# Optimization experiments

Measured on AMD Instinct MI355X. Metric: run time of the kernel, lower is better.

## Reference

```python
import jax, jax.numpy as jnp
import numpy as np

B, L, H, C = 1, 512, 1024, 2


def setup_inputs() -> dict:
    key = jax.random.key(0)
    k1, k2, k3 = jax.random.split(key, 3)
    lm_output = jax.random.normal(k1, (B, L, H), dtype=jnp.float32)
    # torch Linear weight layout: [out_features, in_features]
    W1 = jax.random.normal(k2, (H, 2 * H), dtype=jnp.float32) * 0.02
    b1 = jnp.zeros((H,), dtype=jnp.float32)
    W2 = jax.random.normal(k3, (C, H), dtype=jnp.float32) * 0.02
    b2 = jnp.zeros((C,), dtype=jnp.float32)
    return {"lm_output": lm_output, "W1": W1, "b1": b1, "W2": W2, "b2": b2}


def reference(lm_output, W1, b1, W2, b2):
    # pair_emb[b,i,j] = concat(lm_output[b,j], lm_output[b,i])
    # Linear(concat(a,b)) decomposes: split W1 into the halves acting on each part.
    Wa = W1[:, :H]  # acts on lm_output_a (the j / column token)
    Wb = W1[:, H:]  # acts on lm_output_b (the i / row token)
    a_proj = jnp.einsum('blh,oh->blo', lm_output, Wa)  # [B,L,H]
    b_proj = jnp.einsum('blh,oh->blo', lm_output, Wb)  # [B,L,H]
    # hidden[b,i,j] = tanh(a_proj[b,j] + b_proj[b,i] + b1)   -> [B,L,L,H]
    hidden = jnp.tanh(a_proj[:, None, :, :] + b_proj[:, :, None, :] + b1)
    # Dropout is identity at inference time.
    logits = jnp.einsum('bijh,ch->bijc', hidden, W2) + b2  # [B,L,L,C]
    logits = (logits + jnp.swapaxes(logits, 1, 2)) / 2.0
    return logits
```

## Files before the change

kernel.cpp:

```cpp
#include <hip/hip_runtime.h>
#include <hip/hip_bf16.h>

#define HH 1024
#define LL 512
#define NT 16
#define NTRI 136

typedef __attribute__((ext_vector_type(8))) short bf16x8;
typedef __attribute__((ext_vector_type(4))) float f32x4;

static constexpr float C_EXP = 2.8853900817779268f;

static __device__ __forceinline__ uint4 pack8(float4 a, float4 b) {
    union { uint4 u; __hip_bfloat162 h[4]; } r;
    r.h[0] = __float22bfloat162_rn(make_float2(a.x, a.y));
    r.h[1] = __float22bfloat162_rn(make_float2(a.z, a.w));
    r.h[2] = __float22bfloat162_rn(make_float2(b.x, b.y));
    r.h[3] = __float22bfloat162_rn(make_float2(b.z, b.w));
    return r.u;
}

__global__ __launch_bounds__(256, 4) void proj_mfma_kernel(
    const float* __restrict__ lm, const float* __restrict__ W1,
    const float* __restrict__ b1, float* __restrict__ Ea, float* __restrict__ Eb)
{
    __shared__ ushort As[16][136];
    __shared__ ushort Bs[64][136];

    const int tid  = threadIdx.x;
    const int lane = tid & 63;
    const int w    = tid >> 6;
    const int mbase = blockIdx.y * 16;
    const int nbase = blockIdx.x * 64;
    const int sel  = nbase >> 10;
    const int nrow = nbase & 1023;
    const int wn   = w * 16;

    const int mrow = lane & 15;
    const int q8   = (lane >> 4) * 8;

    f32x4 acc = {0.f, 0.f, 0.f, 0.f};

    for (int kb = 0; kb < HH; kb += 128) {
        __syncthreads();
        {
            const int row = tid >> 4, c8 = (tid & 15) * 8;
            const float* pa = &lm[(mbase + row) * HH + kb + c8];
            *(uint4*)&As[row][c8] = pack8(*(const float4*)pa, *(const float4*)(pa + 4));
            int p = tid;
#pragma unroll
            for (int it = 0; it < 4; ++it, p += 256) {
                const int br = p >> 4, bc8 = (p & 15) * 8;
                const float* pb = &W1[(nrow + br) * 2048 + sel * 1024 + kb + bc8];
                *(uint4*)&Bs[br][bc8] = pack8(*(const float4*)pb, *(const float4*)(pb + 4));
            }
        }
        __syncthreads();

#pragma unroll
        for (int s = 0; s < 4; ++s) {
            const bf16x8 a = *(const bf16x8*)&As[mrow][s * 32 + q8];
            const bf16x8 b = *(const bf16x8*)&Bs[wn + mrow][s * 32 + q8];
            acc = __builtin_amdgcn_mfma_f32_16x16x32_bf16(a, b, acc, 0, 0, 0);
        }
    }

    const int col = lane & 15;
    const int rq  = (lane >> 4) * 4;
    const int n_g = nbase + wn + col;
    const int m0  = mbase + rq;
    if (n_g < HH) {
        const float bb = b1[n_g];
#pragma unroll
        for (int r = 0; r < 4; ++r)
            Ea[(m0 + r) * HH + n_g] = __builtin_amdgcn_exp2f(C_EXP * (acc[r] + bb));
    } else {
#pragma unroll
        for (int r = 0; r < 4; ++r)
            Eb[(m0 + r) * HH + (n_g - HH)] = __builtin_amdgcn_exp2f(C_EXP * acc[r]);
    }
}

__global__ __launch_bounds__(256, 4) void pair_kernel(
    const float* __restrict__ Ea, const float* __restrict__ Eb,
    const float* __restrict__ W2, float* __restrict__ pbuf, int nz)
{
    __shared__ float eaj[32][68];
    __shared__ float eai[32][68];
    __shared__ float ebi[32][68];
    __shared__ float ebj[32][68];
    __shared__ float w0_s[256], w1_s[256];
    __shared__ float s_red[2];

    const int tid = threadIdx.x;
    const int tx  = tid & 15;
    const int ty  = tid >> 4;

    int tt = blockIdx.x, bi = 0, rem = NT;
    while (tt >= rem) { tt -= rem; --rem; ++bi; }
    const int bj    = bi + tt;
    const int ibase = bi * 32;
    const int jbase = bj * 32;
    const int slice = HH / nz;
    const int k0    = blockIdx.y * slice;

    if (tid < 128) {
        const int c = tid >> 6, l = tid & 63;
        float* ws = c ? w1_s : w0_s;
        float s = 0.f;
        for (int q = l; q < slice / 4; q += 64) {
            const float4 v = *(const float4*)&W2[c * HH + k0 + q * 4];
            const float4 nv = make_float4(-2.f * v.x, -2.f * v.y, -2.f * v.z, -2.f * v.w);
            ((float4*)ws)[q] = nv;
            s += nv.x + nv.y + nv.z + nv.w;
        }
#pragma unroll
        for (int off = 32; off; off >>= 1) s += __shfl_down(s, off, 64);
        if (l == 0) s_red[c] = -0.5f * s;
    }

    float acc[2][2][2] = {};

    for (int kb = 0; kb < slice; kb += 64) {
        __syncthreads();
        {
            int p = tid;
#pragma unroll
            for (int it = 0; it < 8; ++it, p += 256) {
                const int tile = p >> 9;
                const int row  = (p >> 4) & 31;
                const int c4   = p & 15;
                float4 v;
                if      (tile == 0) v = *(const float4*)&Ea[(jbase + row) * HH + k0 + kb + c4 * 4];
                else if (tile == 1) v = *(const float4*)&Ea[(ibase + row) * HH + k0 + kb + c4 * 4];
                else if (tile == 2) v = *(const float4*)&Eb[(ibase + row) * HH + k0 + kb + c4 * 4];
                else                v = *(const float4*)&Eb[(jbase + row) * HH + k0 + kb + c4 * 4];
                if      (tile == 0) *(float4*)&eaj[row][c4 * 4] = v;
                else if (tile == 1) *(float4*)&eai[row][c4 * 4] = v;
                else if (tile == 2) *(float4*)&ebi[row][c4 * 4] = v;
                else                *(float4*)&ebj[row][c4 * 4] = v;
            }
        }
        __syncthreads();

#pragma unroll 4
        for (int h4 = 0; h4 < 16; ++h4) {
            const float4 Aj0 = *(const float4*)&eaj[tx][h4 * 4];
            const float4 Aj1 = *(const float4*)&eaj[tx + 16][h4 * 4];
            const float4 Bi0 = *(const float4*)&ebi[ty][h4 * 4];
            const float4 Bi1 = *(const float4*)&ebi[ty + 16][h4 * 4];
            const float4 Ai0 = *(const float4*)&eai[ty][h4 * 4];
            const float4 Ai1 = *(const float4*)&eai[ty + 16][h4 * 4];
            const float4 Bj0 = *(const float4*)&ebj[tx][h4 * 4];
            const float4 Bj1 = *(const float4*)&ebj[tx + 16][h4 * 4];
            const float4 w0  = *(const float4*)&w0_s[kb + h4 * 4];
            const float4 w1  = *(const float4*)&w1_s[kb + h4 * 4];

#define DO_H(AJ0, AJ1, BI0, BI1, AI0, AI1, BJ0, BJ1, W0V, W1V)        \
            {                                                          \
                const float d00 = __builtin_fmaf((BI0), (AJ0), 1.f);   \
                const float d01 = __builtin_fmaf((BI0), (AJ1), 1.f);   \
                const float d10 = __builtin_fmaf((BI1), (AJ0), 1.f);   \
                const float d11 = __builtin_fmaf((BI1), (AJ1), 1.f);   \
                const float e00 = __builtin_fmaf((AI0), (BJ0), 1.f);   \
                const float e01 = __builtin_fmaf((AI0), (BJ1), 1.f);   \
                const float e10 = __builtin_fmaf((AI1), (BJ0), 1.f);   \
                const float e11 = __builtin_fmaf((AI1), (BJ1), 1.f);   \
                const float dp0 = d00 * d01, dp1 = d10 * d11;          \
                const float DR  = __builtin_amdgcn_rcpf(dp0 * dp1);    \
                const float dq0 = DR * dp1, dq1 = DR * dp0;            \
                const float rd00 = dq0 * d01, rd01 = dq0 * d00;        \
                const float rd10 = dq1 * d11, rd11 = dq1 * d10;        \
                const float ep0 = e00 * e01, ep1 = e10 * e11;          \
                const float ER  = __builtin_amdgcn_rcpf(ep0 * ep1);    \
                const float eq0 = ER * ep1, eq1 = ER * ep0;            \
                const float re00 = eq0 * e01, re01 = eq0 * e00;        \
                const float re10 = eq1 * e11, re11 = eq1 * e10;        \
                const float u00 = rd00 + re00, u01 = rd01 + re01;      \
                const float u10 = rd10 + re10, u11 = rd11 + re11;      \
                acc[0][0][0] = __builtin_fmaf(u00, (W0V), acc[0][0][0]); \
                acc[0][0][1] = __builtin_fmaf(u00, (W1V), acc[0][0][1]); \
                acc[0][1][0] = __builtin_fmaf(u01, (W0V), acc[0][1][0]); \
                acc[0][1][1] = __builtin_fmaf(u01, (W1V), acc[0][1][1]); \
                acc[1][0][0] = __builtin_fmaf(u10, (W0V), acc[1][0][0]); \
                acc[1][0][1] = __builtin_fmaf(u10, (W1V), acc[1][0][1]); \
                acc[1][1][0] = __builtin_fmaf(u11, (W0V), acc[1][1][0]); \
                acc[1][1][1] = __builtin_fmaf(u11, (W1V), acc[1][1][1]); \
            }
            DO_H(Aj0.x, Aj1.x, Bi0.x, Bi1.x, Ai0.x, Ai1.x, Bj0.x, Bj1.x, w0.x, w1.x)
            DO_H(Aj0.y, Aj1.y, Bi0.y, Bi1.y, Ai0.y, Ai1.y, Bj0.y, Bj1.y, w0.y, w1.y)
            DO_H(Aj0.z, Aj1.z, Bi0.z, Bi1.z, Ai0.z, Ai1.z, Bj0.z, Bj1.z, w0.z, w1.z)
            DO_H(Aj0.w, Aj1.w, Bi0.w, Bi1.w, Ai0.w, Ai1.w, Bj0.w, Bj1.w, w0.w, w1.w)
#undef DO_H
        }
    }

    const float s0 = s_red[0];
    const float s1 = s_red[1];
    float* pb = pbuf + ((size_t)blockIdx.y * NTRI + blockIdx.x) * 2048;
#pragma unroll
    for (int ii = 0; ii < 2; ++ii) {
#pragma unroll
        for (int jj = 0; jj < 2; ++jj) {
            const int li = ty + ii * 16, lj = tx + jj * 16;
            float2* dst = (float2*)&pb[(li * 32 + lj) * 2];
            *dst = make_float2(0.5f * acc[ii][jj][0] + s0,
                               0.5f * acc[ii][jj][1] + s1);
        }
    }
}

__global__ __launch_bounds__(256) void combine_kernel(
    const float* __restrict__ pbuf, const float* __restrict__ b2,
    float* __restrict__ out, int nz)
{
    const int idx   = blockIdx.x * 256 + threadIdx.x;
    const int t     = idx >> 11;
    const int local = idx & 2047;
    int tt = t, bi = 0, rem = NT;
    while (tt >= rem) { tt -= rem; --rem; ++bi; }
    const int bj = bi + tt;

    float s = 0.f;
    for (int z = 0; z < nz; ++z)
        s += pbuf[((size_t)z * NTRI + t) * 2048 + local];

    const int li = local >> 6;
    const int lj = (local >> 1) & 31;
    const int c  = local & 1;
    s += b2[c];

    const int i = bi * 32 + li;
    const int j = bj * 32 + lj;
    out[(i * LL + j) * 2 + c] = s;
    out[(j * LL + i) * 2 + c] = s;
}

extern "C" void kernel_launch(void* const* d_in, const int* in_sizes, int n_in,
                              void* d_out, int out_size, void* d_ws, size_t ws_size,
                              hipStream_t stream)
{
    const float* lm = (const float*)d_in[0];
    const float* W1 = (const float*)d_in[1];
    const float* b1 = (const float*)d_in[2];
    const float* W2 = (const float*)d_in[3];
    const float* b2 = (const float*)d_in[4];
    float* out = (float*)d_out;

    float* Ea   = (float*)d_ws;
    float* Eb   = Ea + (size_t)LL * HH;
    float* pbuf = Eb + (size_t)LL * HH;

    const size_t base = (size_t)4 * LL * HH * 2;
    int nz = 8;
    while (nz > 1 && base + (size_t)nz * NTRI * 2048 * 4 > ws_size) nz >>= 1;

    proj_mfma_kernel<<<dim3(32, 32), 256, 0, stream>>>(lm, W1, b1, Ea, Eb);
    pair_kernel<<<dim3(NTRI, nz), 256, 0, stream>>>(Ea, Eb, W2, pbuf, nz);
    combine_kernel<<<(NTRI * 2048) / 256, 256, 0, stream>>>(pbuf, b2, out, nz);
}
```

Measured before the change: 137.1 us.

## Pre-convert inputs to bf16, remap proj blocks per XCD, raise split-K count

Adds a conversion kernel that packs lm_output and W1 into bf16 once, so the projection GEMM loads pre-converted tiles instead of repacking fp32 in every block. Projection blocks are remapped so each XCD works on a contiguous group of N tiles. The W2 scaling and sum reduction move out of the pair kernel into the conversion and combine steps. The split-K factor for the pair kernel is raised to 16. These add an extra launch and a larger partial-sum buffer for combine to reduce.

```diff
diff --git a/kernel.cpp b/kernel.cpp
--- a/kernel.cpp
+++ b/kernel.cpp
@@ -20,8 +20,42 @@
     return r.u;
 }
 
+__global__ __launch_bounds__(256) void convert_kernel(
+    const float* __restrict__ lm, const float* __restrict__ W1,
+    const float* __restrict__ W2,
+    ushort* __restrict__ lm16, ushort* __restrict__ B16, float* __restrict__ wsum)
+{
+    const int b = blockIdx.x;
+    if (b == 1280) {
+        const int tid = threadIdx.x;
+        if (tid < 128) {
+            const int c = tid >> 6, l = tid & 63;
+            float s = 0.f;
+            for (int q = l; q < 256; q += 64) {
+                const float4 v = *(const float4*)&W2[c * HH + q * 4];
+                s += v.x + v.y + v.z + v.w;
+            }
+#pragma unroll
+            for (int off = 32; off; off >>= 1) s += __shfl_down(s, off, 64);
+            if (l == 0) wsum[c] = s;
+        }
+        return;
+    }
+    const int q = b * 256 + threadIdx.x;
+    if (q < 65536) {
+        const float4 a = *(const float4*)&lm[q * 8];
+        const float4 c = *(const float4*)&lm[q * 8 + 4];
+        ((uint4*)lm16)[q] = pack8(a, c);
+    } else {
+        const int p = q - 65536;
+        const int n = p >> 7, k8 = (p & 127) * 8;
+        const float* src = &W1[(n & 1023) * 2048 + (n >> 10) * 1024 + k8];
+        ((uint4*)B16)[p] = pack8(*(const float4*)src, *(const float4*)(src + 4));
+    }
+}
+
 __global__ __launch_bounds__(256, 4) void proj_mfma_kernel(
-    const float* __restrict__ lm, const float* __restrict__ W1,
+    const ushort* __restrict__ lm16, const ushort* __restrict__ B16,
     const float* __restrict__ b1, float* __restrict__ Ea, float* __restrict__ Eb)
 {
     __shared__ ushort As[16][136];
@@ -30,10 +64,11 @@
     const int tid  = threadIdx.x;
     const int lane = tid & 63;
     const int w    = tid >> 6;
-    const int mbase = blockIdx.y * 16;
-    const int nbase = blockIdx.x * 64;
-    const int sel  = nbase >> 10;
-    const int nrow = nbase & 1023;
+    const int linear = blockIdx.x;
+    const int xcd  = linear & 7;
+    const int idx  = linear >> 3;
+    const int nbase = (xcd * 4 + (idx & 3)) * 64;
+    const int mbase = (idx >> 2) * 16;
     const int wn   = w * 16;
 
     const int mrow = lane & 15;
@@ -45,14 +80,12 @@
         __syncthreads();
         {
             const int row = tid >> 4, c8 = (tid & 15) * 8;
-            const float* pa = &lm[(mbase + row) * HH + kb + c8];
-            *(uint4*)&As[row][c8] = pack8(*(const float4*)pa, *(const float4*)(pa + 4));
+            *(uint4*)&As[row][c8] = *(const uint4*)&lm16[(mbase + row) * HH + kb + c8];
             int p = tid;
 #pragma unroll
             for (int it = 0; it < 4; ++it, p += 256) {
                 const int br = p >> 4, bc8 = (p & 15) * 8;
-                const float* pb = &W1[(nrow + br) * 2048 + sel * 1024 + kb + bc8];
-                *(uint4*)&Bs[br][bc8] = pack8(*(const float4*)pb, *(const float4*)(pb + 4));
+                *(uint4*)&Bs[br][bc8] = *(const uint4*)&B16[(nbase + br) * HH + kb + bc8];
             }
         }
         __syncthreads();
@@ -90,7 +123,6 @@
     __shared__ float ebi[32][68];
     __shared__ float ebj[32][68];
     __shared__ float w0_s[256], w1_s[256];
-    __shared__ float s_red[2];
 
     const int tid = threadIdx.x;
     const int tx  = tid & 15;
@@ -107,16 +139,8 @@
     if (tid < 128) {
         const int c = tid >> 6, l = tid & 63;
         float* ws = c ? w1_s : w0_s;
-        float s = 0.f;
-        for (int q = l; q < slice / 4; q += 64) {
-            const float4 v = *(const float4*)&W2[c * HH + k0 + q * 4];
-            const float4 nv = make_float4(-2.f * v.x, -2.f * v.y, -2.f * v.z, -2.f * v.w);
-            ((float4*)ws)[q] = nv;
-            s += nv.x + nv.y + nv.z + nv.w;
-        }
-#pragma unroll
-        for (int off = 32; off; off >>= 1) s += __shfl_down(s, off, 64);
-        if (l == 0) s_red[c] = -0.5f * s;
+        for (int q = l; q < slice / 4; q += 64)
+            ((float4*)ws)[q] = *(const float4*)&W2[c * HH + k0 + q * 4];
     }
 
     float acc[2][2][2] = {};
@@ -195,24 +219,20 @@
         }
     }
 
-    const float s0 = s_red[0];
-    const float s1 = s_red[1];
     float* pb = pbuf + ((size_t)blockIdx.y * NTRI + blockIdx.x) * 2048;
 #pragma unroll
-    for (int ii = 0; ii < 2; ++ii) {
+    for (int ii = 0; ii < 2; ++ii)
 #pragma unroll
         for (int jj = 0; jj < 2; ++jj) {
             const int li = ty + ii * 16, lj = tx + jj * 16;
-            float2* dst = (float2*)&pb[(li * 32 + lj) * 2];
-            *dst = make_float2(0.5f * acc[ii][jj][0] + s0,
-                               0.5f * acc[ii][jj][1] + s1);
-        }
-    }
+            *(float2*)&pb[(li * 32 + lj) * 2] =
+                make_float2(acc[ii][jj][0], acc[ii][jj][1]);
+        }
 }
 
 __global__ __launch_bounds__(256) void combine_kernel(
     const float* __restrict__ pbuf, const float* __restrict__ b2,
-    float* __restrict__ out, int nz)
+    const float* __restrict__ wsum, float* __restrict__ out, int nz)
 {
     const int idx   = blockIdx.x * 256 + threadIdx.x;
     const int t     = idx >> 11;
@@ -228,12 +248,12 @@
     const int li = local >> 6;
     const int lj = (local >> 1) & 31;
     const int c  = local & 1;
-    s += b2[c];
+    const float v = wsum[c] + b2[c] - s;
 
     const int i = bi * 32 + li;
     const int j = bj * 32 + lj;
-    out[(i * LL + j) * 2 + c] = s;
-    out[(j * LL + i) * 2 + c] = s;
+    out[(i * LL + j) * 2 + c] = v;
+    out[(j * LL + i) * 2 + c] = v;
 }
 
 extern "C" void kernel_launch(void* const* d_in, const int* in_sizes, int n_in,
@@ -247,15 +267,20 @@
     const float* b2 = (const float*)d_in[4];
     float* out = (float*)d_out;
 
-    float* Ea   = (float*)d_ws;
-    float* Eb   = Ea + (size_t)LL * HH;
-    float* pbuf = Eb + (size_t)LL * HH;
-
-    const size_t base = (size_t)4 * LL * HH * 2;
-    int nz = 8;
-    while (nz > 1 && base + (size_t)nz * NTRI * 2048 * 4 > ws_size) nz >>= 1;
-
-    proj_mfma_kernel<<<dim3(32, 32), 256, 0, stream>>>(lm, W1, b1, Ea, Eb);
+    char* ws = (char*)d_ws;
+    float*  Ea   = (float*)ws;
+    float*  Eb   = (float*)(ws + (2u << 20));
+    ushort* lm16 = (ushort*)(ws + (4u << 20));
+    ushort* B16  = (ushort*)(ws + (5u << 20));
+    float*  wsum = (float*)(ws + (9u << 20));
+    float*  pbuf = (float*)(ws + (9u << 20) + 256);
+
+    const size_t base = (9u << 20) + 256;
+    int nz = 16;
+    while (nz > 4 && base + (size_t)nz * NTRI * 2048 * 4 > ws_size) nz >>= 1;
+
+    convert_kernel<<<1281, 256, 0, stream>>>(lm, W1, W2, lm16, B16, wsum);
+    proj_mfma_kernel<<<1024, 256, 0, stream>>>(lm16, B16, b1, Ea, Eb);
     pair_kernel<<<dim3(NTRI, nz), 256, 0, stream>>>(Ea, Eb, W2, pbuf, nz);
-    combine_kernel<<<(NTRI * 2048) / 256, 256, 0, stream>>>(pbuf, b2, out, nz);
-}
+    combine_kernel<<<(NTRI * 2048) / 256, 256, 0, stream>>>(pbuf, b2, wsum, out, nz);
+}
```

Measured after the change: 130.8 us. 1.05x faster.
